# Optimization experiments

Hardware: AMD Instinct MI355X
Metric: run time of the kernel (lower is better)

Reference implementation:

```python
import jax, jax.numpy as jnp
import numpy as np

N_NODES = 50000
N_EDGES = 800000
D = 64
NUM_LAYERS = 4
NUM_GRAPHS = 128
EPS = 0.0


def setup_inputs() -> dict:
    key = jax.random.key(0)
    ks = jax.random.split(key, 6)
    x = jax.random.normal(ks[0], (N_NODES, D), dtype=jnp.float32)
    edge_index = jax.random.randint(ks[1], (2, N_EDGES), 0, N_NODES, dtype=jnp.int64)
    expander_edge_index = jax.random.randint(ks[2], (2, N_EDGES), 0, N_NODES, dtype=jnp.int64)
    batch = jnp.sort(jax.random.randint(ks[3], (N_NODES,), 0, NUM_GRAPHS, dtype=jnp.int64))
    # Linear params for each GIN layer (all 64->64 here): W [L, out, in], b [L, out]
    Ws = jax.random.normal(ks[4], (NUM_LAYERS, D, D), dtype=jnp.float32) / np.sqrt(D)
    bs = jax.random.normal(ks[5], (NUM_LAYERS, D), dtype=jnp.float32) * 0.01
    return {"x": x, "edge_index": edge_index, "expander_edge_index": expander_edge_index,
            "batch": batch, "Ws": Ws, "bs": bs}


def _gin_agg(x, edge_index):
    # (1+eps)*x_i + sum_{j in N(i)} x_j ; messages flow src->dst
    src, dst = edge_index[0], edge_index[1]
    agg = jax.ops.segment_sum(x[src], dst, num_segments=N_NODES)
    return (1.0 + EPS) * x + agg


def reference(x, edge_index, expander_edge_index, batch, Ws, bs):
    for i in range(NUM_LAYERS):
        # GINConv with Linear nn on real graph
        h = _gin_agg(x, edge_index)                     # [N, D]
        h = h @ Ws[i].T + bs[i]                         # [N, D]
        h = jax.nn.relu(h)
        # GINConv with Identity nn on expander graph
        x = _gin_agg(h, expander_edge_index)            # [N, D]
    pooled = jax.ops.segment_sum(x, batch, num_segments=NUM_GRAPHS)  # [G, D]
    return pooled.reshape(-1)
```

## Files before the change

### kernel.cpp

```cpp
#include <hip/hip_runtime.h>

#define N_NODES 50000
#define N_EDGES 800000
#define D 64
#define NUM_LAYERS 4
#define NUM_GRAPHS 128
#define N_ALL (2 * N_NODES)
#define E_ALL (2 * N_EDGES)
#define BSHIFT 9
#define NBUCK ((N_ALL + 511) / 512)
#define CHUNK 3072
#define NCHUNK ((E_ALL + CHUNK - 1) / CHUNK)

__device__ __forceinline__ unsigned f2bf(float f) {
    unsigned u = __float_as_uint(f);
    return (u + 0x7FFFu + ((u >> 16) & 1u)) >> 16;
}
__device__ __forceinline__ float bflo(unsigned p) { return __uint_as_float(p << 16); }
__device__ __forceinline__ float bfhi(unsigned p) { return __uint_as_float(p & 0xFFFF0000u); }
__device__ __forceinline__ void acc8(float* a, uint4 v) {
    a[0] += bflo(v.x); a[1] += bfhi(v.x);
    a[2] += bflo(v.y); a[3] += bfhi(v.y);
    a[4] += bflo(v.z); a[5] += bfhi(v.z);
    a[6] += bflo(v.w); a[7] += bfhi(v.w);
}

__global__ __launch_bounds__(256) void x_to_bf16(const float4* __restrict__ xf,
                                                 uint4* __restrict__ xb,
                                                 int* __restrict__ bucketTotal) {
    int t = threadIdx.x;
    if (blockIdx.x == 0 && t < NBUCK) bucketTotal[t] = 0;
    int idx = blockIdx.x * 256 + t;
    if (idx < N_NODES * D / 8) {
        float4 v0 = xf[(size_t)idx * 2];
        float4 v1 = xf[(size_t)idx * 2 + 1];
        uint4 o;
        o.x = f2bf(v0.x) | (f2bf(v0.y) << 16);
        o.y = f2bf(v0.z) | (f2bf(v0.w) << 16);
        o.z = f2bf(v1.x) | (f2bf(v1.y) << 16);
        o.w = f2bf(v1.z) | (f2bf(v1.w) << 16);
        xb[idx] = o;
    }
}

#define BC_BLOCKS 256
__global__ __launch_bounds__(256) void bucket_count(const int* __restrict__ dR,
                                                    const int* __restrict__ dX,
                                                    int* __restrict__ bucketTotal) {
    __shared__ int lc[NBUCK];
    int t = threadIdx.x;
    for (int j = t; j < NBUCK; j += 256) lc[j] = 0;
    __syncthreads();
    for (int e = blockIdx.x * 256 + t; e < N_EDGES; e += BC_BLOCKS * 256) {
        atomicAdd(&lc[dR[e] >> BSHIFT], 1);
        atomicAdd(&lc[(N_NODES + dX[e]) >> BSHIFT], 1);
    }
    __syncthreads();
    for (int j = t; j < NBUCK; j += 256) {
        int v = lc[j];
        if (v) atomicAdd(&bucketTotal[j], v);
    }
}

__global__ __launch_bounds__(256) void bucket_scan(const int* __restrict__ bucketTotal,
                                                   int* __restrict__ bucketBase,
                                                   int* __restrict__ bucketCursor) {
    __shared__ int s[256];
    int t = threadIdx.x;
    int v = (t < NBUCK) ? bucketTotal[t] : 0;
    s[t] = v;
    __syncthreads();
    for (int off = 1; off < 256; off <<= 1) {
        int tv = (t >= off) ? s[t - off] : 0;
        __syncthreads();
        s[t] += tv;
        __syncthreads();
    }
    if (t < NBUCK) {
        int excl = s[t] - v;
        bucketBase[t] = excl;
        bucketCursor[t] = excl;
    }
    if (t == NBUCK - 1) bucketBase[NBUCK] = s[t];
}

__global__ __launch_bounds__(256) void bin_scatter(const int* __restrict__ sR,
                                                   const int* __restrict__ dR,
                                                   const int* __restrict__ sX,
                                                   const int* __restrict__ dX,
                                                   int* __restrict__ bucketCursor,
                                                   unsigned* __restrict__ pairs) {
    __shared__ unsigned lpair[CHUNK];
    __shared__ unsigned char lbuck[CHUNK];
    __shared__ int lcnt[NBUCK];
    __shared__ int lbase[NBUCK];
    __shared__ int gbase[NBUCK];
    __shared__ int sc[256];
    __shared__ int tot;
    int t = threadIdx.x;
    for (int j = t; j < NBUCK; j += 256) lcnt[j] = 0;
    __syncthreads();

    int base = blockIdx.x * CHUNK;
    unsigned myp[12];
    int myr[12], myb[12];
#pragma unroll
    for (int i = 0; i < 12; ++i) {
        int e = base + i * 256 + t;
        if (e < E_ALL) {
            bool isR = (e < N_EDGES);
            int d = isR ? dR[e] : (N_NODES + dX[e - N_EDGES]);
            int s = isR ? sR[e] : sX[e - N_EDGES];
            myp[i] = ((unsigned)(d & 511) << 16) | (unsigned)s;
            myb[i] = d >> BSHIFT;
            myr[i] = atomicAdd(&lcnt[myb[i]], 1);
        }
    }
    __syncthreads();

    int v = (t < NBUCK) ? lcnt[t] : 0;
    sc[t] = v;
    __syncthreads();
    for (int off = 1; off < 256; off <<= 1) {
        int tv = (t >= off) ? sc[t - off] : 0;
        __syncthreads();
        sc[t] += tv;
        __syncthreads();
    }
    if (t < NBUCK) {
        lbase[t] = sc[t] - v;
        if (v > 0) gbase[t] = atomicAdd(&bucketCursor[t], v);
    }
    if (t == NBUCK - 1) tot = sc[t];
    __syncthreads();

#pragma unroll
    for (int i = 0; i < 12; ++i) {
        int e = base + i * 256 + t;
        if (e < E_ALL) {
            int p = lbase[myb[i]] + myr[i];
            lpair[p] = myp[i];
            lbuck[p] = (unsigned char)myb[i];
        }
    }
    __syncthreads();

    int total = tot;
    for (int j = t; j < total; j += 256) {
        int b = lbuck[j];
        pairs[(size_t)gbase[b] + (j - lbase[b])] = lpair[j];
    }
}

__global__ __launch_bounds__(256) void bucket_place(const unsigned* __restrict__ pairs,
                                                    const int* __restrict__ bucketBase,
                                                    int* __restrict__ rowptr,
                                                    unsigned short* __restrict__ col) {
    __shared__ unsigned short scol[10240];
    __shared__ int ldeg[512];
    __shared__ int lcur[512];
    __shared__ int s1[256];
    int b = blockIdx.x;
    int d0 = b << BSHIFT;
    int nd = min(512, N_ALL - d0);
    int t = threadIdx.x;
    int base = bucketBase[b];
    int cnt = bucketBase[b + 1] - base;
    ldeg[t] = 0; ldeg[t + 256] = 0;
    __syncthreads();
    for (int i = t; i < cnt; i += 256) {
        int dl = pairs[(size_t)base + i] >> 16;
        atomicAdd(&ldeg[dl], 1);
    }
    __syncthreads();
    int v0 = ldeg[2 * t], v1 = ldeg[2 * t + 1];
    int pv = v0 + v1;
    s1[t] = pv;
    __syncthreads();
    for (int off = 1; off < 256; off <<= 1) {
        int tv = (t >= off) ? s1[t - off] : 0;
        __syncthreads();
        s1[t] += tv;
        __syncthreads();
    }
    int before = s1[t] - pv;
    lcur[2 * t] = before;
    lcur[2 * t + 1] = before + v0;
    if (2 * t < nd)     rowptr[d0 + 2 * t]     = base + before;
    if (2 * t + 1 < nd) rowptr[d0 + 2 * t + 1] = base + before + v0;
    if (b == NBUCK - 1 && t == 0) rowptr[N_ALL] = base + cnt;
    __syncthreads();
    for (int i = t; i < cnt; i += 256) {
        unsigned pr = pairs[(size_t)base + i];
        int dl = pr >> 16;
        int p = atomicAdd(&lcur[dl], 1);
        scol[p] = (unsigned short)(pr & 0xFFFFu);
    }
    __syncthreads();
    for (int i = t; i < cnt; i += 256) col[base + i] = scol[i];
}

__global__ __launch_bounds__(256, 8) void gather_bf16(const uint4* __restrict__ xb,
                                                      uint4* __restrict__ ob,
                                                      const int* __restrict__ rowptr,
                                                      const unsigned short* __restrict__ col) {
    int t = threadIdx.x;
    int grp = t >> 4;
    int half = (t >> 3) & 1;
    int ln8 = t & 7;
    int node = blockIdx.x * 16 + grp;
    int beg = rowptr[node], end = rowptr[node + 1];
    int cnt = end - beg;
    int ch = (cnt - half + 1) >> 1;
    const unsigned short* cp = col + beg + half;
    float a[8];
    if (half == 0) {
        uint4 v = xb[(size_t)node * 8 + ln8];
        a[0] = bflo(v.x); a[1] = bfhi(v.x); a[2] = bflo(v.y); a[3] = bfhi(v.y);
        a[4] = bflo(v.z); a[5] = bfhi(v.z); a[6] = bflo(v.w); a[7] = bfhi(v.w);
    } else {
#pragma unroll
        for (int i = 0; i < 8; ++i) a[i] = 0.0f;
    }
    int i = 0;
    for (; i + 8 <= ch; i += 8) {
        int s0 = cp[2 * i],      s1 = cp[2 * i + 2],  s2 = cp[2 * i + 4],  s3 = cp[2 * i + 6];
        int s4 = cp[2 * i + 8],  s5 = cp[2 * i + 10], s6 = cp[2 * i + 12], s7 = cp[2 * i + 14];
        uint4 v0 = xb[(size_t)s0 * 8 + ln8];
        uint4 v1 = xb[(size_t)s1 * 8 + ln8];
        uint4 v2 = xb[(size_t)s2 * 8 + ln8];
        uint4 v3 = xb[(size_t)s3 * 8 + ln8];
        uint4 v4 = xb[(size_t)s4 * 8 + ln8];
        uint4 v5 = xb[(size_t)s5 * 8 + ln8];
        uint4 v6 = xb[(size_t)s6 * 8 + ln8];
        uint4 v7 = xb[(size_t)s7 * 8 + ln8];
        acc8(a, v0); acc8(a, v1); acc8(a, v2); acc8(a, v3);
        acc8(a, v4); acc8(a, v5); acc8(a, v6); acc8(a, v7);
    }
    for (; i + 4 <= ch; i += 4) {
        int s0 = cp[2 * i], s1 = cp[2 * i + 2], s2 = cp[2 * i + 4], s3 = cp[2 * i + 6];
        uint4 v0 = xb[(size_t)s0 * 8 + ln8];
        uint4 v1 = xb[(size_t)s1 * 8 + ln8];
        uint4 v2 = xb[(size_t)s2 * 8 + ln8];
        uint4 v3 = xb[(size_t)s3 * 8 + ln8];
        acc8(a, v0); acc8(a, v1); acc8(a, v2); acc8(a, v3);
    }
    for (; i < ch; ++i) acc8(a, xb[(size_t)cp[2 * i] * 8 + ln8]);
#pragma unroll
    for (int j = 0; j < 8; ++j) a[j] += __shfl_xor(a[j], 8);
    if (half == 0) {
        uint4 o;
        o.x = f2bf(a[0]) | (f2bf(a[1]) << 16);
        o.y = f2bf(a[2]) | (f2bf(a[3]) << 16);
        o.z = f2bf(a[4]) | (f2bf(a[5]) << 16);
        o.w = f2bf(a[6]) | (f2bf(a[7]) << 16);
        ob[(size_t)node * 8 + ln8] = o;
    }
}

__global__ __launch_bounds__(256, 6) void gather_linear(const uint4* __restrict__ xb,
                                                        unsigned short* __restrict__ y,
                                                        const int* __restrict__ rowptr,
                                                        const unsigned short* __restrict__ col,
                                                        const float* __restrict__ W,
                                                        const float* __restrict__ b) {
    __shared__ float Wl[64 * 65];
    __shared__ float hl[16 * 64];
    int t = threadIdx.x;
#pragma unroll
    for (int i = 0; i < 16; ++i) {
        int idx = i * 256 + t;
        Wl[(idx >> 6) * 65 + (idx & 63)] = W[idx];
    }
    int grp = t >> 4;
    int node = blockIdx.x * 16 + grp;
    int beg = rowptr[node], end = rowptr[node + 1];
    int half = (t >> 3) & 1;
    int ln8 = t & 7;
    int cnt = end - beg;
    int ch = (cnt - half + 1) >> 1;
    const unsigned short* cp = col + beg + half;
    float a[8];
    if (half == 0) {
        uint4 v = xb[(size_t)node * 8 + ln8];
        a[0] = bflo(v.x); a[1] = bfhi(v.x); a[2] = bflo(v.y); a[3] = bfhi(v.y);
        a[4] = bflo(v.z); a[5] = bfhi(v.z); a[6] = bflo(v.w); a[7] = bfhi(v.w);
    } else {
#pragma unroll
        for (int i = 0; i < 8; ++i) a[i] = 0.0f;
    }
    int i = 0;
    for (; i + 8 <= ch; i += 8) {
        int s0 = cp[2 * i],      s1 = cp[2 * i + 2],  s2 = cp[2 * i + 4],  s3 = cp[2 * i + 6];
        int s4 = cp[2 * i + 8],  s5 = cp[2 * i + 10], s6 = cp[2 * i + 12], s7 = cp[2 * i + 14];
        uint4 v0 = xb[(size_t)s0 * 8 + ln8];
        uint4 v1 = xb[(size_t)s1 * 8 + ln8];
        uint4 v2 = xb[(size_t)s2 * 8 + ln8];
        uint4 v3 = xb[(size_t)s3 * 8 + ln8];
        uint4 v4 = xb[(size_t)s4 * 8 + ln8];
        uint4 v5 = xb[(size_t)s5 * 8 + ln8];
        uint4 v6 = xb[(size_t)s6 * 8 + ln8];
        uint4 v7 = xb[(size_t)s7 * 8 + ln8];
        acc8(a, v0); acc8(a, v1); acc8(a, v2); acc8(a, v3);
        acc8(a, v4); acc8(a, v5); acc8(a, v6); acc8(a, v7);
    }
    for (; i + 4 <= ch; i += 4) {
        int s0 = cp[2 * i], s1 = cp[2 * i + 2], s2 = cp[2 * i + 4], s3 = cp[2 * i + 6];
        uint4 v0 = xb[(size_t)s0 * 8 + ln8];
        uint4 v1 = xb[(size_t)s1 * 8 + ln8];
        uint4 v2 = xb[(size_t)s2 * 8 + ln8];
        uint4 v3 = xb[(size_t)s3 * 8 + ln8];
        acc8(a, v0); acc8(a, v1); acc8(a, v2); acc8(a, v3);
    }
    for (; i < ch; ++i) acc8(a, xb[(size_t)cp[2 * i] * 8 + ln8]);
#pragma unroll
    for (int j = 0; j < 8; ++j) a[j] += __shfl_xor(a[j], 8);
    if (half == 0) {
        float4* hp = (float4*)(hl + grp * 64 + ln8 * 8);
        hp[0] = make_float4(a[0], a[1], a[2], a[3]);
        hp[1] = make_float4(a[4], a[5], a[6], a[7]);
    }
    __syncthreads();

    int o = t & 63, nb = t >> 6;
    float bo = b[o];
    float a0 = bo, a1 = bo, a2 = bo, a3 = bo;
#pragma unroll
    for (int k = 0; k < 64; ++k) {
        float w = Wl[o * 65 + k];
        a0 += hl[(nb     ) * 64 + k] * w;
        a1 += hl[(nb +  4) * 64 + k] * w;
        a2 += hl[(nb +  8) * 64 + k] * w;
        a3 += hl[(nb + 12) * 64 + k] * w;
    }
    size_t base = (size_t)blockIdx.x * 16;
    y[(base + nb     ) * 64 + o] = (unsigned short)f2bf(fmaxf(a0, 0.0f));
    y[(base + nb +  4) * 64 + o] = (unsigned short)f2bf(fmaxf(a1, 0.0f));
    y[(base + nb +  8) * 64 + o] = (unsigned short)f2bf(fmaxf(a2, 0.0f));
    y[(base + nb + 12) * 64 + o] = (unsigned short)f2bf(fmaxf(a3, 0.0f));
}

__device__ __forceinline__ int lower_bound_dev(const int* __restrict__ a, int n, int v) {
    int lo = 0, hi = n;
    while (lo < hi) { int mid = (lo + hi) >> 1; if (a[mid] < v) lo = mid + 1; else hi = mid; }
    return lo;
}

__global__ __launch_bounds__(256) void pool_seg_bf16(const unsigned short* __restrict__ xb,
                                                     const int* __restrict__ batch,
                                                     float* __restrict__ out) {
    int g = blockIdx.x;
    int lo = lower_bound_dev(batch, N_NODES, g);
    int hi = lower_bound_dev(batch, N_NODES, g + 1);
    int lane = threadIdx.x & 63;
    int sub = threadIdx.x >> 6;
    float acc = 0.0f;
    for (int n = lo + sub; n < hi; n += 4)
        acc += __uint_as_float(((unsigned)xb[(size_t)n * 64 + lane]) << 16);
    __shared__ float red[256];
    red[threadIdx.x] = acc;
    __syncthreads();
    if (sub == 0)
        out[(size_t)g * D + lane] = red[lane] + red[64 + lane] + red[128 + lane] + red[192 + lane];
}

extern "C" void kernel_launch(void* const* d_in, const int* in_sizes, int n_in,
                              void* d_out, int out_size, void* d_ws, size_t ws_size,
                              hipStream_t stream) {
    const float* x_in  = (const float*)d_in[0];
    const int*   ei    = (const int*)d_in[1];
    const int*   eei   = (const int*)d_in[2];
    const int*   batch = (const int*)d_in[3];
    const float* Ws    = (const float*)d_in[4];
    const float* bs    = (const float*)d_in[5];
    float* out = (float*)d_out;

    unsigned short* A = (unsigned short*)d_ws;
    unsigned short* B = A + (size_t)N_NODES * D;
    unsigned short* colAll = B + (size_t)N_NODES * D;
    unsigned* pairs = (unsigned*)(colAll + E_ALL);
    int* p = (int*)(pairs + E_ALL);
    int* rowptr = p;        p += N_ALL + 1;
    int* bucketTotal = p;   p += NBUCK;
    int* bucketBase = p;    p += NBUCK + 1;
    int* bucketCursor = p;  p += NBUCK;

    const int* e_src = ei;
    const int* e_dst = ei + N_EDGES;
    const int* x_src = eei;
    const int* x_dst = eei + N_EDGES;

    dim3 blk(256);

    const int cgrid = (N_NODES * D / 8 + 255) / 256;
    x_to_bf16<<<cgrid, blk, 0, stream>>>((const float4*)x_in, (uint4*)B, bucketTotal);

    bucket_count<<<BC_BLOCKS, blk, 0, stream>>>(e_dst, x_dst, bucketTotal);
    bucket_scan<<<1, blk, 0, stream>>>(bucketTotal, bucketBase, bucketCursor);
    bin_scatter<<<NCHUNK, blk, 0, stream>>>(e_src, e_dst, x_src, x_dst, bucketCursor, pairs);
    bucket_place<<<NBUCK, blk, 0, stream>>>(pairs, bucketBase, rowptr, colAll);

    const int lgrid = N_NODES / 16;

    for (int i = 0; i < NUM_LAYERS; ++i) {
        gather_linear<<<lgrid, blk, 0, stream>>>((const uint4*)B, A,
                                                 rowptr, colAll,
                                                 Ws + (size_t)i * D * D,
                                                 bs + (size_t)i * D);
        gather_bf16<<<lgrid, blk, 0, stream>>>((const uint4*)A, (uint4*)B,
                                               rowptr + N_NODES, colAll);
    }

    pool_seg_bf16<<<NUM_GRAPHS, blk, 0, stream>>>(B, batch, out);
}
```

Baseline: 316.0 us.

## Sort nodes by in-degree to balance gather workload across blocks

Builds a degree histogram during CSR construction, then a counting-sort permutation that orders destination nodes by descending degree, separately for the real and expander graphs. The gather kernels process nodes in this permuted order so each 16-node block holds nodes of similar degree, which reduces divergence and tail imbalance inside blocks. In exchange it adds two small kernels, one extra indirection per node, and scattered output writes that lose the contiguous row layout of the original stores.

```diff
diff --git a/kernel.cpp b/kernel.cpp
--- a/kernel.cpp
+++ b/kernel.cpp
@@ -27,9 +27,11 @@
 
 __global__ __launch_bounds__(256) void x_to_bf16(const float4* __restrict__ xf,
                                                  uint4* __restrict__ xb,
-                                                 int* __restrict__ bucketTotal) {
+                                                 int* __restrict__ bucketTotal,
+                                                 int* __restrict__ degHist) {
     int t = threadIdx.x;
     if (blockIdx.x == 0 && t < NBUCK) bucketTotal[t] = 0;
+    if (blockIdx.x == 1 && t < 128) degHist[t] = 0;
     int idx = blockIdx.x * 256 + t;
     if (idx < N_NODES * D / 8) {
         float4 v0 = xf[(size_t)idx * 2];
@@ -155,11 +157,13 @@
 __global__ __launch_bounds__(256) void bucket_place(const unsigned* __restrict__ pairs,
                                                     const int* __restrict__ bucketBase,
                                                     int* __restrict__ rowptr,
-                                                    unsigned short* __restrict__ col) {
+                                                    unsigned short* __restrict__ col,
+                                                    int* __restrict__ degHist) {
     __shared__ unsigned short scol[10240];
     __shared__ int ldeg[512];
     __shared__ int lcur[512];
     __shared__ int s1[256];
+    __shared__ int dh[128];
     int b = blockIdx.x;
     int d0 = b << BSHIFT;
     int nd = min(512, N_ALL - d0);
@@ -167,6 +171,7 @@
     int base = bucketBase[b];
     int cnt = bucketBase[b + 1] - base;
     ldeg[t] = 0; ldeg[t + 256] = 0;
+    if (t < 128) dh[t] = 0;
     __syncthreads();
     for (int i = t; i < cnt; i += 256) {
         int dl = pairs[(size_t)base + i] >> 16;
@@ -186,8 +191,15 @@
     int before = s1[t] - pv;
     lcur[2 * t] = before;
     lcur[2 * t + 1] = before + v0;
-    if (2 * t < nd)     rowptr[d0 + 2 * t]     = base + before;
-    if (2 * t + 1 < nd) rowptr[d0 + 2 * t + 1] = base + before + v0;
+    int n0 = d0 + 2 * t, n1 = d0 + 2 * t + 1;
+    if (2 * t < nd) {
+        rowptr[n0] = base + before;
+        atomicAdd(&dh[min(v0, 63) + ((n0 < N_NODES) ? 0 : 64)], 1);
+    }
+    if (2 * t + 1 < nd) {
+        rowptr[n1] = base + before + v0;
+        atomicAdd(&dh[min(v1, 63) + ((n1 < N_NODES) ? 0 : 64)], 1);
+    }
     if (b == NBUCK - 1 && t == 0) rowptr[N_ALL] = base + cnt;
     __syncthreads();
     for (int i = t; i < cnt; i += 256) {
@@ -198,17 +210,64 @@
     }
     __syncthreads();
     for (int i = t; i < cnt; i += 256) col[base + i] = scol[i];
+    if (t < 128 && dh[t]) atomicAdd(&degHist[t], dh[t]);
+}
+
+__global__ __launch_bounds__(128) void perm_scan(const int* __restrict__ degHist,
+                                                 int* __restrict__ permCursor) {
+    int t = threadIdx.x;
+    int half = t >> 6;
+    int bin = t & 63;
+    int base = half * 64;
+    int sum = 0;
+    for (int b2 = bin + 1; b2 < 64; ++b2) sum += degHist[base + b2];
+    permCursor[t] = sum;
+}
+
+__global__ __launch_bounds__(256) void perm_scatter(const int* __restrict__ rowptr,
+                                                    int* __restrict__ permCursor,
+                                                    int* __restrict__ permR,
+                                                    int* __restrict__ permX) {
+    __shared__ int lc[128], lb[128];
+    int t = threadIdx.x;
+    if (t < 128) lc[t] = 0;
+    __syncthreads();
+    int bins[2], ranks[2];
+#pragma unroll
+    for (int k = 0; k < 2; ++k) {
+        int n = blockIdx.x * 512 + t + k * 256;
+        bins[k] = -1;
+        if (n < N_ALL) {
+            int deg = rowptr[n + 1] - rowptr[n];
+            int bin = min(deg, 63) + ((n < N_NODES) ? 0 : 64);
+            bins[k] = bin;
+            ranks[k] = atomicAdd(&lc[bin], 1);
+        }
+    }
+    __syncthreads();
+    if (t < 128 && lc[t]) lb[t] = atomicAdd(&permCursor[t], lc[t]);
+    __syncthreads();
+#pragma unroll
+    for (int k = 0; k < 2; ++k) {
+        if (bins[k] >= 0) {
+            int n = blockIdx.x * 512 + t + k * 256;
+            int pos = lb[bins[k]] + ranks[k];
+            if (bins[k] < 64) permR[pos] = n;
+            else permX[pos] = n - N_NODES;
+        }
+    }
 }
 
 __global__ __launch_bounds__(256, 8) void gather_bf16(const uint4* __restrict__ xb,
                                                       uint4* __restrict__ ob,
                                                       const int* __restrict__ rowptr,
-                                                      const unsigned short* __restrict__ col) {
+                                                      const unsigned short* __restrict__ col,
+                                                      const int* __restrict__ perm) {
     int t = threadIdx.x;
     int grp = t >> 4;
     int half = (t >> 3) & 1;
     int ln8 = t & 7;
-    int node = blockIdx.x * 16 + grp;
+    int node = perm[blockIdx.x * 16 + grp];
     int beg = rowptr[node], end = rowptr[node + 1];
     int cnt = end - beg;
     int ch = (cnt - half + 1) >> 1;
@@ -263,9 +322,11 @@
                                                         const int* __restrict__ rowptr,
                                                         const unsigned short* __restrict__ col,
                                                         const float* __restrict__ W,
-                                                        const float* __restrict__ b) {
+                                                        const float* __restrict__ b,
+                                                        const int* __restrict__ perm) {
     __shared__ float Wl[64 * 65];
     __shared__ float hl[16 * 64];
+    __shared__ int ids[16];
     int t = threadIdx.x;
 #pragma unroll
     for (int i = 0; i < 16; ++i) {
@@ -273,7 +334,8 @@
         Wl[(idx >> 6) * 65 + (idx & 63)] = W[idx];
     }
     int grp = t >> 4;
-    int node = blockIdx.x * 16 + grp;
+    int node = perm[blockIdx.x * 16 + grp];
+    if ((t & 15) == 0) ids[grp] = node;
     int beg = rowptr[node], end = rowptr[node + 1];
     int half = (t >> 3) & 1;
     int ln8 = t & 7;
@@ -333,11 +395,11 @@
         a2 += hl[(nb +  8) * 64 + k] * w;
         a3 += hl[(nb + 12) * 64 + k] * w;
     }
-    size_t base = (size_t)blockIdx.x * 16;
-    y[(base + nb     ) * 64 + o] = (unsigned short)f2bf(fmaxf(a0, 0.0f));
-    y[(base + nb +  4) * 64 + o] = (unsigned short)f2bf(fmaxf(a1, 0.0f));
-    y[(base + nb +  8) * 64 + o] = (unsigned short)f2bf(fmaxf(a2, 0.0f));
-    y[(base + nb + 12) * 64 + o] = (unsigned short)f2bf(fmaxf(a3, 0.0f));
+    int r0 = ids[nb], r1 = ids[nb + 4], r2 = ids[nb + 8], r3 = ids[nb + 12];
+    y[(size_t)r0 * 64 + o] = (unsigned short)f2bf(fmaxf(a0, 0.0f));
+    y[(size_t)r1 * 64 + o] = (unsigned short)f2bf(fmaxf(a1, 0.0f));
+    y[(size_t)r2 * 64 + o] = (unsigned short)f2bf(fmaxf(a2, 0.0f));
+    y[(size_t)r3 * 64 + o] = (unsigned short)f2bf(fmaxf(a3, 0.0f));
 }
 
 __device__ __forceinline__ int lower_bound_dev(const int* __restrict__ a, int n, int v) {
@@ -384,6 +446,10 @@
     int* bucketTotal = p;   p += NBUCK;
     int* bucketBase = p;    p += NBUCK + 1;
     int* bucketCursor = p;  p += NBUCK;
+    int* degHist = p;       p += 128;
+    int* permCursor = p;    p += 128;
+    int* permR = p;         p += N_NODES;
+    int* permX = p;         p += N_NODES;
 
     const int* e_src = ei;
     const int* e_dst = ei + N_EDGES;
@@ -393,12 +459,15 @@
     dim3 blk(256);
 
     const int cgrid = (N_NODES * D / 8 + 255) / 256;
-    x_to_bf16<<<cgrid, blk, 0, stream>>>((const float4*)x_in, (uint4*)B, bucketTotal);
+    x_to_bf16<<<cgrid, blk, 0, stream>>>((const float4*)x_in, (uint4*)B, bucketTotal, degHist);
 
     bucket_count<<<BC_BLOCKS, blk, 0, stream>>>(e_dst, x_dst, bucketTotal);
     bucket_scan<<<1, blk, 0, stream>>>(bucketTotal, bucketBase, bucketCursor);
     bin_scatter<<<NCHUNK, blk, 0, stream>>>(e_src, e_dst, x_src, x_dst, bucketCursor, pairs);
-    bucket_place<<<NBUCK, blk, 0, stream>>>(pairs, bucketBase, rowptr, colAll);
+    bucket_place<<<NBUCK, blk, 0, stream>>>(pairs, bucketBase, rowptr, colAll, degHist);
+
+    perm_scan<<<1, dim3(128), 0, stream>>>(degHist, permCursor);
+    perm_scatter<<<NBUCK, blk, 0, stream>>>(rowptr, permCursor, permR, permX);
 
     const int lgrid = N_NODES / 16;
 
@@ -406,9 +475,11 @@
         gather_linear<<<lgrid, blk, 0, stream>>>((const uint4*)B, A,
                                                  rowptr, colAll,
                                                  Ws + (size_t)i * D * D,
-                                                 bs + (size_t)i * D);
+                                                 bs + (size_t)i * D,
+                                                 permR);
         gather_bf16<<<lgrid, blk, 0, stream>>>((const uint4*)A, (uint4*)B,
-                                               rowptr + N_NODES, colAll);
+                                               rowptr + N_NODES, colAll,
+                                               permX);
     }
 
     pool_seg_bf16<<<NUM_GRAPHS, blk, 0, stream>>>(B, batch, out);
```

Measured after the change: 318.9 us. No clear change (+0.9%).
